# Kernel tuning notes

Hardware: AMD Instinct MI355X
Metric: run time of the kernel (lower is better)

Reference implementation:

```python
import jax, jax.numpy as jnp
import numpy as np

P_SCALE = 5.0
Q_SCALE = 0.3
EPS = 1e-06
NORM_EPS = 1e-12


def stack3x3_same(img):
    """im2col for 3x3 kernel, 'same' zero padding, stride 1.
    img: (B,H,W,C) -> (B,H,W,9,C), tap order row-major (dy,dx) in {-1,0,1}^2,
    matching the TF stack3x3 ordering with clip=0, pad=1."""
    B, H, W, C = img.shape
    padded = jnp.pad(img, ((0, 0), (1, 1), (1, 1), (0, 0)))
    taps = [padded[:, dy:dy + H, dx:dx + W, :] for dy in range(3) for dx in range(3)]
    return jnp.stack(taps, axis=3)


def setup_inputs() -> dict:
    key = jax.random.key(0)
    k1, k2 = jax.random.split(key)
    B, H, W, C = 32, 64, 64, 64
    n_kernels, ksize = 128, 3
    inputs = jax.random.normal(k1, (B, H, W, C), dtype=jnp.float32)
    # glorot-uniform-ish weight, shape (1, C*k*k, n_kernels)
    fan_in = C * ksize * ksize
    limit = np.sqrt(6.0 / (fan_in + n_kernels)).astype(np.float32)
    w = jax.random.uniform(k2, (1, fan_in, n_kernels), dtype=jnp.float32,
                           minval=-limit, maxval=limit)
    p = jnp.full((n_kernels,), 0.7 * P_SCALE, dtype=jnp.float32)
    q = jnp.full((1,), 1.0 * Q_SCALE, dtype=jnp.float32)
    return {"inputs": inputs, "w": w, "p": p, "q": q}


def reference(inputs, w, p, q):
    B, H, W, C = inputs.shape
    n_kernels = w.shape[-1]
    ksq = w.shape[1] // C  # kernel_size^2 = 9

    # im2col: (B, H*W, C*9), tap-major flatten (matches tf stack axis=3 + reshape)
    x = stack3x3_same(inputs).reshape(B, H * W, ksq * C)

    p_eff = jnp.exp(p / P_SCALE)            # (n_kernels,)
    q_eff = jnp.exp(-q / Q_SCALE)           # (1,)

    # L2 norms (sqrt of clamped square-sum), matching l2_normal
    x_norm = jnp.sqrt(jnp.maximum(jnp.sum(x * x, axis=2, keepdims=True), NORM_EPS)) + q_eff
    w_norm = jnp.sqrt(jnp.maximum(jnp.sum(w * w, axis=1, keepdims=True), NORM_EPS))

    # cosine-similarity matmul: (B, HW, K) x (1, K, N) -> (B, HW, N)
    sim = jnp.einsum('bsk,kn->bsn', x / x_norm, (w / w_norm)[0])

    # sharpened rescaling: sign(x) * (|x| + eps)^p
    out = jnp.sign(sim) * jnp.power(jnp.abs(sim) + EPS, p_eff)
    return out.reshape(B, H, W, n_kernels)
```

## Files before the change

kernel.cpp:

```cpp
#include <hip/hip_runtime.h>
#include <hip/hip_bf16.h>


typedef short bf16x8 __attribute__((ext_vector_type(8)));
typedef float f32x4 __attribute__((ext_vector_type(4)));

__device__ __forceinline__ unsigned short f2bf(float f) {
    union { float f; unsigned int u; } v; v.f = f;
    unsigned int u = v.u;
    unsigned int r = (u + 0x7fffu + ((u >> 16) & 1u)) >> 16;
    return (unsigned short)r;
}

__global__ void prep_w_kernel(const float* __restrict__ w,
                              unsigned short* __restrict__ wn2) {
    const int n = blockIdx.x;
    const int lane = threadIdx.x;
    float vals[9];
    float s = 0.f;
#pragma unroll
    for (int i = 0; i < 9; ++i) {
        float v = w[(i * 64 + lane) * 128 + n];
        vals[i] = v;
        s += v * v;
    }
#pragma unroll
    for (int off = 1; off < 64; off <<= 1) s += __shfl_xor(s, off);
    const float inv = 1.0f / sqrtf(fmaxf(s, 1e-12f));
    const int kc = lane >> 5, koff = lane & 31;
#pragma unroll
    for (int i = 0; i < 9; ++i)
        wn2[((i * 2 + kc) * 128 + n) * 32 + koff] = f2bf(vals[i] * inv);
}

__global__ __launch_bounds__(256, 4) void cossim_main(
    const float* __restrict__ in, const unsigned short* __restrict__ wn,
    const float* __restrict__ p, const float* __restrict__ q,
    float* __restrict__ out) {
    __shared__ unsigned short A[4 * 66 * 72];
    __shared__ float rcsum[256];
    __shared__ float xni[128];
    __shared__ float pfs[128];

    const int tid = (int)threadIdx.x;
    const int l = ((int)blockIdx.x & 7) * 128 + ((int)blockIdx.x >> 3);
    const int b = l >> 5, y0 = (l & 31) * 2;

    if (tid < 128) pfs[tid] = expf(p[tid] * 0.2f);

    {
        const int r = tid >> 6;
        const int col = tid & 63;
        const int row = y0 + r - 1;
        unsigned short* dst = &A[(r * 66 + col + 1) * 72];
        float s = 0.f;
        if ((unsigned)row < 64u) {
            const float4* src = reinterpret_cast<const float4*>(
                in + (size_t)b * 262144 + row * 4096 + col * 64);
#pragma unroll
            for (int it = 0; it < 8; ++it) {
                float4 v0 = src[2 * it];
                float4 v1 = src[2 * it + 1];
                s += v0.x * v0.x + v0.y * v0.y + v0.z * v0.z + v0.w * v0.w;
                s += v1.x * v1.x + v1.y * v1.y + v1.z * v1.z + v1.w * v1.w;
                union { float f; unsigned u; } ux, uy, uz, uw;
                uint4 pk;
                ux.f = v0.x; uy.f = v0.y; uz.f = v0.z; uw.f = v0.w;
                pk.x = __builtin_amdgcn_perm(uy.u + 0x8000u, ux.u + 0x8000u, 0x07060302u);
                pk.y = __builtin_amdgcn_perm(uw.u + 0x8000u, uz.u + 0x8000u, 0x07060302u);
                ux.f = v1.x; uy.f = v1.y; uz.f = v1.z; uw.f = v1.w;
                pk.z = __builtin_amdgcn_perm(uy.u + 0x8000u, ux.u + 0x8000u, 0x07060302u);
                pk.w = __builtin_amdgcn_perm(uw.u + 0x8000u, uz.u + 0x8000u, 0x07060302u);
                *reinterpret_cast<uint4*>(dst + it * 8) = pk;
            }
        } else {
            uint4 z; z.x = z.y = z.z = z.w = 0u;
#pragma unroll
            for (int it = 0; it < 8; ++it)
                *reinterpret_cast<uint4*>(dst + it * 8) = z;
        }
        rcsum[tid] = s;
    }
    if (tid < 64) {
        const int r = tid >> 4, side = (tid >> 3) & 1, ch = (tid & 7) * 8;
        uint4 z; z.x = z.y = z.z = z.w = 0u;
        *reinterpret_cast<uint4*>(&A[(r * 66 + side * 65) * 72 + ch]) = z;
    }
    __syncthreads();

    if (tid < 128) {
        const int ry = tid >> 6, x = tid & 63;
        const float qe = expf(q[0] * (-1.0f / 0.3f));
        float s = 0.f;
#pragma unroll
        for (int dy = 0; dy < 3; ++dy) {
            const float* rs = &rcsum[(ry + dy) * 64];
            if (x > 0) s += rs[x - 1];
            s += rs[x];
            if (x < 63) s += rs[x + 1];
        }
        xni[tid] = 1.0f / (sqrtf(fmaxf(s, 1e-12f)) + qe);
    }

    const int wv = tid >> 6, lane = tid & 63;
    const int lr = lane & 15, lg = lane >> 4;
    const int wm = wv >> 1, wnh = wv & 1;
    f32x4 acc[4][4] = {};
    const unsigned short* wB = wn + (wnh * 64 + lr) * 32 + lg * 8;

#pragma unroll
    for (int dy = 0; dy < 3; ++dy) {
#pragma unroll
        for (int dx = 0; dx < 3; ++dx) {
            const int tap = dy * 3 + dx;
#pragma unroll
            for (int kc = 0; kc < 2; ++kc) {
                const unsigned short* wt = wB + (tap * 2 + kc) * 4096;
                bf16x8 b0 = *reinterpret_cast<const bf16x8*>(wt);
                bf16x8 b1 = *reinterpret_cast<const bf16x8*>(wt + 512);
                bf16x8 b2 = *reinterpret_cast<const bf16x8*>(wt + 1024);
                bf16x8 b3 = *reinterpret_cast<const bf16x8*>(wt + 1536);
                const unsigned short* abase =
                    &A[((wm + dy) * 66 + lr + dx) * 72 + kc * 32 + lg * 8];
#pragma unroll
                for (int mf = 0; mf < 4; ++mf) {
                    bf16x8 av = *reinterpret_cast<const bf16x8*>(abase + mf * 16 * 72);
                    acc[mf][0] = __builtin_amdgcn_mfma_f32_16x16x32_bf16(av, b0, acc[mf][0], 0, 0, 0);
                    acc[mf][1] = __builtin_amdgcn_mfma_f32_16x16x32_bf16(av, b1, acc[mf][1], 0, 0, 0);
                    acc[mf][2] = __builtin_amdgcn_mfma_f32_16x16x32_bf16(av, b2, acc[mf][2], 0, 0, 0);
                    acc[mf][3] = __builtin_amdgcn_mfma_f32_16x16x32_bf16(av, b3, acc[mf][3], 0, 0, 0);
                }
            }
        }
    }
    __syncthreads();

    float* orow = out + ((size_t)(b * 64 + y0 + wm) * 64) * 128;
#pragma unroll
    for (int mf = 0; mf < 4; ++mf) {
#pragma unroll
        for (int i = 0; i < 4; ++i) {
            const int pix = mf * 16 + lg * 4 + i;
            const float xn = xni[wm * 64 + pix];
#pragma unroll
            for (int nf = 0; nf < 4; ++nf) {
                const int n = wnh * 64 + nf * 16 + lr;
                float sim = acc[mf][nf][i] * xn;
                float aa = fabsf(sim) + 1e-6f;
                float r = exp2f(pfs[n] * log2f(aa));
                orow[(size_t)pix * 128 + n] = copysignf(r, sim);
            }
        }
    }
}

extern "C" void kernel_launch(void* const* d_in, const int* in_sizes, int n_in,
                              void* d_out, int out_size, void* d_ws, size_t ws_size,
                              hipStream_t stream) {
    (void)in_sizes; (void)n_in; (void)out_size; (void)ws_size;
    const float* in = (const float*)d_in[0];
    const float* w  = (const float*)d_in[1];
    const float* p  = (const float*)d_in[2];
    const float* q  = (const float*)d_in[3];
    float* out = (float*)d_out;
    unsigned short* wn = (unsigned short*)d_ws;

    prep_w_kernel<<<128, 64, 0, stream>>>(w, wn);
    cossim_main<<<1024, 256, 0, stream>>>(in, wn, p, q, out);
}
```

Measured before the change: 45.71 us.

## Process four output rows per block with prefetched halo rows in a ring buffer

Each block now computes four output rows in two phases instead of two. The input rows needed by the second phase are loaded into registers before the first MFMA phase and written into a 5-slot LDS ring afterward, so the load latency overlaps compute. This cuts halo re-reads of input rows (6 rows per 4 outputs instead of 4 per 2) and halves the grid. In exchange it uses more LDS and registers (launch bounds drop to 2 blocks per CU) and adds a serialized second phase per block.

```diff
diff --git a/kernel.cpp b/kernel.cpp
--- a/kernel.cpp
+++ b/kernel.cpp
@@ -33,18 +33,21 @@
         wn2[((i * 2 + kc) * 128 + n) * 32 + koff] = f2bf(vals[i] * inv);
 }
 
-__global__ __launch_bounds__(256, 4) void cossim_main(
+#define SLOT 4752
+__global__ __launch_bounds__(256, 2) void cossim_main(
     const float* __restrict__ in, const unsigned short* __restrict__ wn,
     const float* __restrict__ p, const float* __restrict__ q,
     float* __restrict__ out) {
-    __shared__ unsigned short A[4 * 66 * 72];
+    __shared__ unsigned short A[5 * 66 * 72];
     __shared__ float rcsum[256];
+    __shared__ float rcj[256];
     __shared__ float xni[128];
     __shared__ float pfs[128];
 
     const int tid = (int)threadIdx.x;
-    const int l = ((int)blockIdx.x & 7) * 128 + ((int)blockIdx.x >> 3);
-    const int b = l >> 5, y0 = (l & 31) * 2;
+    const int l = ((int)blockIdx.x & 7) * 64 + ((int)blockIdx.x >> 3);
+    const int b = l >> 4, y0 = (l & 15) * 4;
+    const float* inb = in + (size_t)b * 262144;
 
     if (tid < 128) pfs[tid] = expf(p[tid] * 0.2f);
 
@@ -52,11 +55,10 @@
         const int r = tid >> 6;
         const int col = tid & 63;
         const int row = y0 + r - 1;
-        unsigned short* dst = &A[(r * 66 + col + 1) * 72];
+        unsigned short* dst = &A[r * SLOT + (col + 1) * 72];
         float s = 0.f;
         if ((unsigned)row < 64u) {
-            const float4* src = reinterpret_cast<const float4*>(
-                in + (size_t)b * 262144 + row * 4096 + col * 64);
+            const float4* src = reinterpret_cast<const float4*>(inb + row * 4096 + col * 64);
 #pragma unroll
             for (int it = 0; it < 8; ++it) {
                 float4 v0 = src[2 * it];
@@ -81,12 +83,26 @@
         }
         rcsum[tid] = s;
     }
-    if (tid < 64) {
+    if (tid < 80) {
         const int r = tid >> 4, side = (tid >> 3) & 1, ch = (tid & 7) * 8;
         uint4 z; z.x = z.y = z.z = z.w = 0u;
-        *reinterpret_cast<uint4*>(&A[(r * 66 + side * 65) * 72 + ch]) = z;
+        *reinterpret_cast<uint4*>(&A[r * SLOT + side * 65 * 72 + ch]) = z;
     }
     __syncthreads();
+
+    const int jhalf = tid >> 7, jt = tid & 127;
+    const int jr = jt >> 6, jcol = jt & 63;
+    const int jrow = y0 + 3 + jr;
+    float4 jv[8];
+    if ((unsigned)jrow < 64u) {
+        const float4* jsrc = reinterpret_cast<const float4*>(
+            inb + jrow * 4096 + jcol * 64 + jhalf * 32);
+#pragma unroll
+        for (int i = 0; i < 8; ++i) jv[i] = jsrc[i];
+    } else {
+#pragma unroll
+        for (int i = 0; i < 8; ++i) jv[i] = make_float4(0.f, 0.f, 0.f, 0.f);
+    }
 
     if (tid < 128) {
         const int ry = tid >> 6, x = tid & 63;
@@ -105,50 +121,145 @@
     const int wv = tid >> 6, lane = tid & 63;
     const int lr = lane & 15, lg = lane >> 4;
     const int wm = wv >> 1, wnh = wv & 1;
-    f32x4 acc[4][4] = {};
     const unsigned short* wB = wn + (wnh * 64 + lr) * 32 + lg * 8;
 
-#pragma unroll
-    for (int dy = 0; dy < 3; ++dy) {
-#pragma unroll
-        for (int dx = 0; dx < 3; ++dx) {
-            const int tap = dy * 3 + dx;
-#pragma unroll
-            for (int kc = 0; kc < 2; ++kc) {
-                const unsigned short* wt = wB + (tap * 2 + kc) * 4096;
-                bf16x8 b0 = *reinterpret_cast<const bf16x8*>(wt);
-                bf16x8 b1 = *reinterpret_cast<const bf16x8*>(wt + 512);
-                bf16x8 b2 = *reinterpret_cast<const bf16x8*>(wt + 1024);
-                bf16x8 b3 = *reinterpret_cast<const bf16x8*>(wt + 1536);
-                const unsigned short* abase =
-                    &A[((wm + dy) * 66 + lr + dx) * 72 + kc * 32 + lg * 8];
-#pragma unroll
-                for (int mf = 0; mf < 4; ++mf) {
-                    bf16x8 av = *reinterpret_cast<const bf16x8*>(abase + mf * 16 * 72);
-                    acc[mf][0] = __builtin_amdgcn_mfma_f32_16x16x32_bf16(av, b0, acc[mf][0], 0, 0, 0);
-                    acc[mf][1] = __builtin_amdgcn_mfma_f32_16x16x32_bf16(av, b1, acc[mf][1], 0, 0, 0);
-                    acc[mf][2] = __builtin_amdgcn_mfma_f32_16x16x32_bf16(av, b2, acc[mf][2], 0, 0, 0);
-                    acc[mf][3] = __builtin_amdgcn_mfma_f32_16x16x32_bf16(av, b3, acc[mf][3], 0, 0, 0);
-                }
-            }
+    {
+        f32x4 acc[4][4] = {};
+#pragma unroll
+        for (int dy = 0; dy < 3; ++dy) {
+#pragma unroll
+            for (int dx = 0; dx < 3; ++dx) {
+                const int tap = dy * 3 + dx;
+#pragma unroll
+                for (int kc = 0; kc < 2; ++kc) {
+                    const unsigned short* wt = wB + (tap * 2 + kc) * 4096;
+                    bf16x8 b0 = *reinterpret_cast<const bf16x8*>(wt);
+                    bf16x8 b1 = *reinterpret_cast<const bf16x8*>(wt + 512);
+                    bf16x8 b2 = *reinterpret_cast<const bf16x8*>(wt + 1024);
+                    bf16x8 b3 = *reinterpret_cast<const bf16x8*>(wt + 1536);
+                    const unsigned short* abase =
+                        &A[(wm + dy) * SLOT + (lr + dx) * 72 + kc * 32 + lg * 8];
+#pragma unroll
+                    for (int mf = 0; mf < 4; ++mf) {
+                        bf16x8 av = *reinterpret_cast<const bf16x8*>(abase + mf * 16 * 72);
+                        acc[mf][0] = __builtin_amdgcn_mfma_f32_16x16x32_bf16(av, b0, acc[mf][0], 0, 0, 0);
+                        acc[mf][1] = __builtin_amdgcn_mfma_f32_16x16x32_bf16(av, b1, acc[mf][1], 0, 0, 0);
+                        acc[mf][2] = __builtin_amdgcn_mfma_f32_16x16x32_bf16(av, b2, acc[mf][2], 0, 0, 0);
+                        acc[mf][3] = __builtin_amdgcn_mfma_f32_16x16x32_bf16(av, b3, acc[mf][3], 0, 0, 0);
+                    }
+                }
+            }
+        }
+        __syncthreads();
+        float* orow = out + ((size_t)(b * 64 + y0 + wm) * 64) * 128;
+#pragma unroll
+        for (int mf = 0; mf < 4; ++mf) {
+#pragma unroll
+            for (int i = 0; i < 4; ++i) {
+                const int pix = mf * 16 + lg * 4 + i;
+                const float xn = xni[wm * 64 + pix];
+#pragma unroll
+                for (int nf = 0; nf < 4; ++nf) {
+                    const int n = wnh * 64 + nf * 16 + lr;
+                    float sim = acc[mf][nf][i] * xn;
+                    float aa = fabsf(sim) + 1e-6f;
+                    float r = exp2f(pfs[n] * log2f(aa));
+                    orow[(size_t)pix * 128 + n] = copysignf(r, sim);
+                }
+            }
+        }
+    }
+
+    {
+        float s = 0.f;
+#pragma unroll
+        for (int i = 0; i < 8; ++i)
+            s += jv[i].x * jv[i].x + jv[i].y * jv[i].y + jv[i].z * jv[i].z + jv[i].w * jv[i].w;
+        rcj[tid] = s;
+        const int slot = jr ? 0 : 4;
+        unsigned short* dst = &A[slot * SLOT + (jcol + 1) * 72 + jhalf * 32];
+#pragma unroll
+        for (int i = 0; i < 4; ++i) {
+            union { float f; unsigned u; } ux, uy, uz, uw;
+            uint4 pk;
+            float4 v0 = jv[2 * i], v1 = jv[2 * i + 1];
+            ux.f = v0.x; uy.f = v0.y; uz.f = v0.z; uw.f = v0.w;
+            pk.x = __builtin_amdgcn_perm(uy.u + 0x8000u, ux.u + 0x8000u, 0x07060302u);
+            pk.y = __builtin_amdgcn_perm(uw.u + 0x8000u, uz.u + 0x8000u, 0x07060302u);
+            ux.f = v1.x; uy.f = v1.y; uz.f = v1.z; uw.f = v1.w;
+            pk.z = __builtin_amdgcn_perm(uy.u + 0x8000u, ux.u + 0x8000u, 0x07060302u);
+            pk.w = __builtin_amdgcn_perm(uw.u + 0x8000u, uz.u + 0x8000u, 0x07060302u);
+            *reinterpret_cast<uint4*>(dst + i * 8) = pk;
         }
     }
     __syncthreads();
 
-    float* orow = out + ((size_t)(b * 64 + y0 + wm) * 64) * 128;
-#pragma unroll
-    for (int mf = 0; mf < 4; ++mf) {
-#pragma unroll
-        for (int i = 0; i < 4; ++i) {
-            const int pix = mf * 16 + lg * 4 + i;
-            const float xn = xni[wm * 64 + pix];
-#pragma unroll
-            for (int nf = 0; nf < 4; ++nf) {
-                const int n = wnh * 64 + nf * 16 + lr;
-                float sim = acc[mf][nf][i] * xn;
-                float aa = fabsf(sim) + 1e-6f;
-                float r = exp2f(pfs[n] * log2f(aa));
-                orow[(size_t)pix * 128 + n] = copysignf(r, sim);
+    if (tid < 128) {
+        const int ry = tid >> 6, x = tid & 63;
+        const float qe = expf(q[0] * (-1.0f / 0.3f));
+        float s = 0.f;
+#pragma unroll
+        for (int dy = 0; dy < 3; ++dy) {
+            const int idx = ry + dy;
+#pragma unroll
+            for (int dc = -1; dc <= 1; ++dc) {
+                const int c = x + dc;
+                if ((unsigned)c < 64u) {
+                    float rs;
+                    if (idx < 2) rs = rcsum[(idx + 2) * 64 + c];
+                    else rs = rcj[(idx - 2) * 64 + c] + rcj[128 + (idx - 2) * 64 + c];
+                    s += rs;
+                }
+            }
+        }
+        xni[tid] = 1.0f / (sqrtf(fmaxf(s, 1e-12f)) + qe);
+    }
+
+    {
+        f32x4 acc[4][4] = {};
+#pragma unroll
+        for (int dy = 0; dy < 3; ++dy) {
+#pragma unroll
+            for (int dx = 0; dx < 3; ++dx) {
+                const int tap = dy * 3 + dx;
+#pragma unroll
+                for (int kc = 0; kc < 2; ++kc) {
+                    const unsigned short* wt = wB + (tap * 2 + kc) * 4096;
+                    bf16x8 b0 = *reinterpret_cast<const bf16x8*>(wt);
+                    bf16x8 b1 = *reinterpret_cast<const bf16x8*>(wt + 512);
+                    bf16x8 b2 = *reinterpret_cast<const bf16x8*>(wt + 1024);
+                    bf16x8 b3 = *reinterpret_cast<const bf16x8*>(wt + 1536);
+                    int srow = wm + dy + 2;
+                    srow = (srow >= 5) ? (srow - 5) : srow;
+                    const unsigned short* abase =
+                        &A[srow * SLOT + (lr + dx) * 72 + kc * 32 + lg * 8];
+#pragma unroll
+                    for (int mf = 0; mf < 4; ++mf) {
+                        bf16x8 av = *reinterpret_cast<const bf16x8*>(abase + mf * 16 * 72);
+                        acc[mf][0] = __builtin_amdgcn_mfma_f32_16x16x32_bf16(av, b0, acc[mf][0], 0, 0, 0);
+                        acc[mf][1] = __builtin_amdgcn_mfma_f32_16x16x32_bf16(av, b1, acc[mf][1], 0, 0, 0);
+                        acc[mf][2] = __builtin_amdgcn_mfma_f32_16x16x32_bf16(av, b2, acc[mf][2], 0, 0, 0);
+                        acc[mf][3] = __builtin_amdgcn_mfma_f32_16x16x32_bf16(av, b3, acc[mf][3], 0, 0, 0);
+                    }
+                }
+            }
+        }
+        __syncthreads();
+        float* orow = out + ((size_t)(b * 64 + y0 + 2 + wm) * 64) * 128;
+#pragma unroll
+        for (int mf = 0; mf < 4; ++mf) {
+#pragma unroll
+            for (int i = 0; i < 4; ++i) {
+                const int pix = mf * 16 + lg * 4 + i;
+                const float xn = xni[wm * 64 + pix];
+#pragma unroll
+                for (int nf = 0; nf < 4; ++nf) {
+                    const int n = wnh * 64 + nf * 16 + lr;
+                    float sim = acc[mf][nf][i] * xn;
+                    float aa = fabsf(sim) + 1e-6f;
+                    float r = exp2f(pfs[n] * log2f(aa));
+                    orow[(size_t)pix * 128 + n] = copysignf(r, sim);
+                }
             }
         }
     }
@@ -166,5 +277,5 @@
     unsigned short* wn = (unsigned short*)d_ws;
 
     prep_w_kernel<<<128, 64, 0, stream>>>(w, wn);
-    cossim_main<<<1024, 256, 0, stream>>>(in, wn, p, q, out);
-}
+    cossim_main<<<512, 256, 0, stream>>>(in, wn, p, q, out);
+}
```

Result: slower. 49.64 us (+8.6%).
